# Kernel optimization log

Measured on AMD Instinct MI355X. Metric: run time of the kernel, lower is better.

Reference implementation:

```python
import jax, jax.numpy as jnp
import numpy as np

N = 50000      # nodes
E = 800000     # edges (avg degree 16)
D = 128        # d_model
C = 2          # num_classes
F_IN = 8       # GCNConv(8, d_model)


def setup_inputs() -> dict:
    key = jax.random.key(0)
    ks = jax.random.split(key, 12)
    s = 0.05  # weight init scale
    return {
        "feature_vec": jax.random.normal(ks[0], (N, F_IN), dtype=jnp.float32),
        "bboxes": jax.random.uniform(ks[1], (N, 4), dtype=jnp.float32),
        "bbox_indices": jnp.arange(N, dtype=jnp.int64) if jax.config.jax_enable_x64 else jnp.arange(N, dtype=jnp.int32),
        "edge_index": jax.random.randint(ks[2], (2, E), 0, N, dtype=jnp.int32),
        "W1": jax.random.normal(ks[3], (F_IN, D), dtype=jnp.float32) * s,
        "b1": jnp.zeros((D,), dtype=jnp.float32),
        "W2": jax.random.normal(ks[4], (D, D), dtype=jnp.float32) * s,
        "b2": jnp.zeros((D,), dtype=jnp.float32),
        "lin1_W": jax.random.normal(ks[5], (2 * D, D), dtype=jnp.float32) * s,
        "lin1_b": jnp.zeros((D,), dtype=jnp.float32),
        "linf_W": jax.random.normal(ks[6], (D, C), dtype=jnp.float32) * s,
        "linf_b": jnp.zeros((C,), dtype=jnp.float32),
    }


def gcn_conv(x, W, b, edge_index, n):
    """PyG GCNConv: add self-loops, symmetric D^-1/2 A D^-1/2 normalization."""
    x = x @ W                                   # [n, out]
    sl = jnp.arange(n, dtype=edge_index.dtype)
    row = jnp.concatenate([edge_index[0], sl])  # source
    col = jnp.concatenate([edge_index[1], sl])  # target
    ones = jnp.ones(row.shape[0], dtype=x.dtype)
    deg = jax.ops.segment_sum(ones, col, num_segments=n)  # >= 1 due to self-loops
    dinv = jax.lax.rsqrt(deg)
    norm = dinv[row] * dinv[col]                # [E + n]
    msg = x[row] * norm[:, None]                # gather + scale
    out = jax.ops.segment_sum(msg, col, num_segments=n)   # scatter-aggregate
    return out + b


def reference(feature_vec, bboxes, bbox_indices, edge_index,
              W1, b1, W2, b2, lin1_W, lin1_b, linf_W, linf_b):
    n = feature_vec.shape[0]
    x = jax.nn.relu(gcn_conv(feature_vec, W1, b1, edge_index, n))
    x = jax.nn.relu(gcn_conv(x, W2, b2, edge_index, n))
    x1 = x[edge_index[0]]                        # [E, D]
    x2 = x[edge_index[1]]                        # [E, D]
    xpair = jnp.concatenate([x1, x2], axis=-1)   # [E, 2D]
    xpair = jax.nn.relu(xpair @ lin1_W + lin1_b)
    xfin = xpair @ linf_W + linf_b               # [E, C]
    probs = jax.nn.log_softmax(xfin, axis=-1)
    bbox_pairs = jnp.concatenate([bboxes[edge_index[0]], bboxes[edge_index[1]]], axis=-1)  # [E, 8]
    bbox_index_pairs = jnp.stack([bbox_indices[edge_index[0]], bbox_indices[edge_index[1]]], axis=1)  # [E, 2]
    return (probs, bbox_pairs, bbox_index_pairs)
```

## Files before the change

kernel.cpp:

```cpp
#include <hip/hip_runtime.h>
#include <hip/hip_bf16.h>
#include <math.h>


typedef __attribute__((ext_vector_type(8))) short short8;
typedef __attribute__((ext_vector_type(4))) float f32x4;
typedef __attribute__((ext_vector_type(2))) float fv2;

__device__ inline ushort f2bf(float f) {
    union { __hip_bfloat16 h; ushort u; } cv;
    cv.h = __float2bfloat16(f);
    return cv.u;
}
__device__ inline float bf2f(ushort u) {
    union { float f; uint u; } c;
    c.u = ((uint)u) << 16;
    return c.f;
}
__device__ inline uchar f2fp8(float f) {
    uint p = __builtin_amdgcn_cvt_pk_fp8_f32(f, f, 0u, false);
    return (uchar)(p & 0xffu);
}

__global__ void k_hist(const int* __restrict__ col, int* __restrict__ cnt, int E) {
    int e = blockIdx.x * blockDim.x + threadIdx.x;
    if (e < E) atomicAdd(&cnt[col[e]], 1);
}

__global__ __launch_bounds__(1024) void k_bsum(const int* __restrict__ cnt,
                                               int* __restrict__ bsum, int N) {
    __shared__ int ts[1024];
    const int b = blockIdx.x, t = threadIdx.x;
    const int i0 = b * 2048 + 2 * t;
    int a0 = (i0 < N) ? cnt[i0] : 0;
    int a1 = (i0 + 1 < N) ? cnt[i0 + 1] : 0;
    ts[t] = a0 + a1;
    __syncthreads();
#pragma unroll
    for (int off = 512; off > 0; off >>= 1) {
        if (t < off) ts[t] += ts[t + off];
        __syncthreads();
    }
    if (t == 0) bsum[b] = ts[0];
}

__global__ __launch_bounds__(1024) void k_scanw(const int* __restrict__ cnt,
                                                const int* __restrict__ bsum,
                                                int* __restrict__ ptr, int N, int E) {
    __shared__ int ts[1024];
    const int b = blockIdx.x, t = threadIdx.x;
    int boff = 0;
    for (int i = 0; i < b; ++i) boff += bsum[i];
    const int i0 = b * 2048 + 2 * t;
    const int a0 = (i0 < N) ? cnt[i0] : 0;
    const int a1 = (i0 + 1 < N) ? cnt[i0 + 1] : 0;
    const int s = a0 + a1;
    ts[t] = s;
    __syncthreads();
    for (int off = 1; off < 1024; off <<= 1) {
        int v = (t >= off) ? ts[t - off] : 0;
        __syncthreads();
        ts[t] += v;
        __syncthreads();
    }
    const int excl = boff + ts[t] - s;
    if (i0 < N) ptr[i0] = excl;
    if (i0 + 1 < N) ptr[i0 + 1] = excl + a0;
    if (b == 0 && t == 0) ptr[N] = E;
}

__global__ void k_fill(const int* __restrict__ row, const int* __restrict__ col,
                       const int* __restrict__ cnt, const int* __restrict__ ptr,
                       int* __restrict__ cursor, int2* __restrict__ eadj, int E) {
    int e = blockIdx.x * blockDim.x + threadIdx.x;
    if (e >= E) return;
    int r = row[e], c = col[e];
    float dr = rsqrtf(1.0f + (float)cnt[r]);
    float dc = rsqrtf(1.0f + (float)cnt[c]);
    int p = ptr[c] + atomicAdd(&cursor[c], 1);
    eadj[p] = make_int2(r, __float_as_int(dr * dc));
}

__global__ void k_prepW(const float* __restrict__ lin1W, const float* __restrict__ W2,
                        ushort* __restrict__ Wuv, ushort* __restrict__ W2t) {
    int tid = blockIdx.x * blockDim.x + threadIdx.x;
    if (tid < 256 * 128) {
        int c = tid >> 7, k = tid & 127;
        int krow = k + ((c >> 7) << 7);
        Wuv[tid] = f2bf(lin1W[krow * 128 + (c & 127)]);
    } else if (tid < 256 * 128 + 128 * 128) {
        int u = tid - 256 * 128;
        int n = u >> 7, k = u & 127;
        W2t[u] = f2bf(W2[k * 128 + n]);
    }
}

__global__ __launch_bounds__(256) void k_l1(const float* __restrict__ feat,
                                            const int* __restrict__ cnt,
                                            const int* __restrict__ ptr,
                                            const int2* __restrict__ eadj,
                                            const float* __restrict__ W1,
                                            const float* __restrict__ b1,
                                            ushort* __restrict__ x1, int N) {
    __shared__ float sagg[32][8];
    __shared__ float sW1[8 * 128];
    const int tid = threadIdx.x;
    for (int i = tid; i < 1024; i += 256) sW1[i] = W1[i];

    const int lane8 = tid & 7;
    const int nloc = tid >> 3;
    const int node = blockIdx.x * 32 + nloc;
    float acc = 0.f;
    if (node < N) {
        float dd = 1.0f / (1.0f + (float)cnt[node]);
        acc = feat[(size_t)node * 8 + lane8] * dd;
        int i = ptr[node], end = ptr[node + 1];
        for (; i < end; ++i) {
            const int2 a = eadj[i];
            acc += feat[(size_t)a.x * 8 + lane8] * __int_as_float(a.y);
        }
    }
    sagg[nloc][lane8] = acc;
    __syncthreads();

    if (node < N) {
        const int jb = lane8 * 16;
        float av[8];
#pragma unroll
        for (int k = 0; k < 8; ++k) av[k] = sagg[nloc][k];
        short8 r0, r1;
#pragma unroll
        for (int j = 0; j < 16; ++j) {
            float s = b1[jb + j];
#pragma unroll
            for (int k = 0; k < 8; ++k) s = fmaf(av[k], sW1[k * 128 + jb + j], s);
            const ushort bv = f2bf(fmaxf(s, 0.f));
            if (j < 8) r0[j] = (short)bv; else r1[j - 8] = (short)bv;
        }
        *reinterpret_cast<short8*>(&x1[(size_t)node * 128 + jb]) = r0;
        *reinterpret_cast<short8*>(&x1[(size_t)node * 128 + jb + 8]) = r1;
    }
}

__global__ __launch_bounds__(256) void k_gemm2(const ushort* __restrict__ x1,
                                               const ushort* __restrict__ W2t,
                                               uchar* __restrict__ h2, int N) {
    __shared__ ushort ldsW[128 * 128];
    const int tid = threadIdx.x;
    const int wave = tid >> 6, lane = tid & 63;
    const int m = lane & 15, kb = lane >> 4;
    const int n0 = blockIdx.x * 64;

    const int node_a = min(n0 + wave * 16 + m, N - 1);
    short8 a[4];
#pragma unroll
    for (int kk = 0; kk < 4; ++kk) {
        a[kk] = *reinterpret_cast<const short8*>(&x1[(size_t)node_a * 128 + kk * 32 + kb * 8]);
    }

    {
        char* lb = reinterpret_cast<char*>(ldsW);
        const short8* wg = reinterpret_cast<const short8*>(W2t);
#pragma unroll
        for (int i = 0; i < 8; ++i) {
            const int g = i * 256 + tid;
            const int bo = g * 16;
            const int swz = bo ^ (((bo >> 8) & 7) << 4);
            *reinterpret_cast<short8*>(lb + swz) = wg[g];
        }
    }
    __syncthreads();

    f32x4 acc[8];
#pragma unroll
    for (int t = 0; t < 8; ++t) acc[t] = (f32x4){0.f, 0.f, 0.f, 0.f};

    const char* lbr = reinterpret_cast<const char*>(ldsW);
    const int mswz = (m & 7) << 4;
#pragma unroll
    for (int kk = 0; kk < 4; ++kk) {
#pragma unroll
        for (int t = 0; t < 8; ++t) {
            const int bo = (t * 16 + m) * 256 + kk * 64 + kb * 16;
            const short8 b = *reinterpret_cast<const short8*>(lbr + (bo ^ mswz));
            acc[t] = __builtin_amdgcn_mfma_f32_16x16x32_bf16(a[kk], b, acc[t], 0, 0, 0);
        }
    }

#pragma unroll
    for (int r = 0; r < 4; ++r) {
        const int node = n0 + wave * 16 + kb * 4 + r;
        if (node < N) {
#pragma unroll
            for (int t = 0; t < 8; ++t) {
                h2[(size_t)node * 128 + t * 16 + m] = f2fp8(acc[t][r]);
            }
        }
    }
}

__global__ __launch_bounds__(256) void k_gather2(const uchar* __restrict__ h2,
                                                 const int* __restrict__ cnt,
                                                 const int* __restrict__ ptr,
                                                 const int2* __restrict__ eadj,
                                                 const float* __restrict__ b2,
                                                 ushort* __restrict__ xbf, int N) {
    const int lane8 = threadIdx.x & 7;
    const int node = blockIdx.x * 32 + (threadIdx.x >> 3);
    if (node >= N) return;
    const float dd = 1.0f / (1.0f + (float)cnt[node]);
    float acc[16];
    {
        const uint4 w = *reinterpret_cast<const uint4*>(&h2[(size_t)node * 128 + lane8 * 16]);
        const uint ws[4] = {w.x, w.y, w.z, w.w};
#pragma unroll
        for (int q = 0; q < 4; ++q) {
            const fv2 lo = __builtin_amdgcn_cvt_pk_f32_fp8(ws[q], false);
            const fv2 hi = __builtin_amdgcn_cvt_pk_f32_fp8(ws[q], true);
            acc[4 * q + 0] = lo[0] * dd;
            acc[4 * q + 1] = lo[1] * dd;
            acc[4 * q + 2] = hi[0] * dd;
            acc[4 * q + 3] = hi[1] * dd;
        }
    }
    int i = ptr[node];
    const int end = ptr[node + 1];
    for (; i < end; ++i) {
        const int2 aa = eadj[i];
        const float nm = __int_as_float(aa.y);
        const uint4 w = *reinterpret_cast<const uint4*>(&h2[(size_t)aa.x * 128 + lane8 * 16]);
        const uint ws[4] = {w.x, w.y, w.z, w.w};
#pragma unroll
        for (int q = 0; q < 4; ++q) {
            const fv2 lo = __builtin_amdgcn_cvt_pk_f32_fp8(ws[q], false);
            const fv2 hi = __builtin_amdgcn_cvt_pk_f32_fp8(ws[q], true);
            acc[4 * q + 0] = fmaf(lo[0], nm, acc[4 * q + 0]);
            acc[4 * q + 1] = fmaf(lo[1], nm, acc[4 * q + 1]);
            acc[4 * q + 2] = fmaf(hi[0], nm, acc[4 * q + 2]);
            acc[4 * q + 3] = fmaf(hi[1], nm, acc[4 * q + 3]);
        }
    }
    short8 r0, r1;
#pragma unroll
    for (int q = 0; q < 8; ++q) {
        r0[q] = (short)f2bf(fmaxf(acc[q] + b2[lane8 * 16 + q], 0.f));
        r1[q] = (short)f2bf(fmaxf(acc[8 + q] + b2[lane8 * 16 + 8 + q], 0.f));
    }
    *reinterpret_cast<short8*>(&xbf[(size_t)node * 128 + lane8 * 16]) = r0;
    *reinterpret_cast<short8*>(&xbf[(size_t)node * 128 + lane8 * 16 + 8]) = r1;
}

__global__ __launch_bounds__(512) void k_gemm_uv(const ushort* __restrict__ xbf,
                                                 const ushort* __restrict__ Wuv,
                                                 const float* __restrict__ lin1b,
                                                 uchar* __restrict__ uv, int N) {
    __shared__ ushort ldsW[256 * 128];
    const int tid = threadIdx.x;
    const int wave = tid >> 6, lane = tid & 63;
    const int m = lane & 15, kb = lane >> 4;
    const int n0 = blockIdx.x * 128 + wave * 16;

    const int node_a = min(n0 + m, N - 1);
    short8 a[4];
#pragma unroll
    for (int kk = 0; kk < 4; ++kk) {
        a[kk] = *reinterpret_cast<const short8*>(&xbf[(size_t)node_a * 128 + kk * 32 + kb * 8]);
    }

    {
        char* lb = reinterpret_cast<char*>(ldsW);
        const short8* wg = reinterpret_cast<const short8*>(Wuv);
#pragma unroll
        for (int i = 0; i < 8; ++i) {
            const int g = i * 512 + tid;
            const int bo = g * 16;
            const int swz = bo ^ (((bo >> 8) & 7) << 4);
            *reinterpret_cast<short8*>(lb + swz) = wg[g];
        }
    }
    __syncthreads();

    const char* lbr = reinterpret_cast<const char*>(ldsW);
    const int mswz = (m & 7) << 4;

#pragma unroll
    for (int ch = 0; ch < 2; ++ch) {
        f32x4 acc[8];
#pragma unroll
        for (int t = 0; t < 8; ++t) acc[t] = (f32x4){0.f, 0.f, 0.f, 0.f};
#pragma unroll
        for (int kk = 0; kk < 4; ++kk) {
#pragma unroll
            for (int t = 0; t < 8; ++t) {
                const int bo = (ch * 128 + t * 16 + m) * 256 + kk * 64 + kb * 16;
                const short8 b = *reinterpret_cast<const short8*>(lbr + (bo ^ mswz));
                acc[t] = __builtin_amdgcn_mfma_f32_16x16x32_bf16(a[kk], b, acc[t], 0, 0, 0);
            }
        }
#pragma unroll
        for (int r = 0; r < 4; ++r) {
            const int node = n0 + kb * 4 + r;
            if (node < N) {
#pragma unroll
                for (int t = 0; t < 8; ++t) {
                    const int c = t * 16 + m;
                    float av = acc[t][r];
                    if (ch == 0) av += lin1b[c];
                    uv[(size_t)node * 256 + ch * 128 + c] = f2fp8(av);
                }
            }
        }
    }
}

__global__ __launch_bounds__(256) void k_edge_lite(const uchar* __restrict__ uv,
                                                   const float* __restrict__ linfW,
                                                   const float* __restrict__ linfb,
                                                   const float* __restrict__ bboxes,
                                                   const int* __restrict__ bidx,
                                                   const int* __restrict__ row,
                                                   const int* __restrict__ col,
                                                   float* __restrict__ out_probs,
                                                   float* __restrict__ out_bbox,
                                                   float* __restrict__ out_bidx,
                                                   int E) {
    const int lane8 = threadIdx.x & 7;
    const int slot = threadIdx.x >> 3;
    int e = blockIdx.x * 32 + slot;
    if (e >= E) return;

    float wd[16];
#pragma unroll
    for (int j = 0; j < 16; ++j) {
        const int c = lane8 * 16 + j;
        wd[j] = linfW[c * 2] - linfW[c * 2 + 1];
    }
    const float bias_d = linfb[0] - linfb[1];
    const int step = gridDim.x * 32;

    int s = row[e], d = col[e];
    uint4 ua = *reinterpret_cast<const uint4*>(&uv[(size_t)s * 256 + lane8 * 16]);
    uint4 va = *reinterpret_cast<const uint4*>(&uv[(size_t)d * 256 + 128 + lane8 * 16]);

    while (true) {
        const int e2 = e + step;
        const bool more = (e2 < E);
        int s2 = 0, d2 = 0;
        uint4 ua2 = ua, va2 = va;
        if (more) {
            s2 = row[e2];
            d2 = col[e2];
            ua2 = *reinterpret_cast<const uint4*>(&uv[(size_t)s2 * 256 + lane8 * 16]);
            va2 = *reinterpret_cast<const uint4*>(&uv[(size_t)d2 * 256 + 128 + lane8 * 16]);
        }

        float p = 0.f;
        {
            const uint uw[4] = {ua.x, ua.y, ua.z, ua.w};
            const uint vw[4] = {va.x, va.y, va.z, va.w};
#pragma unroll
            for (int w = 0; w < 4; ++w) {
                const fv2 ul = __builtin_amdgcn_cvt_pk_f32_fp8(uw[w], false);
                const fv2 uh = __builtin_amdgcn_cvt_pk_f32_fp8(uw[w], true);
                const fv2 vl = __builtin_amdgcn_cvt_pk_f32_fp8(vw[w], false);
                const fv2 vh = __builtin_amdgcn_cvt_pk_f32_fp8(vw[w], true);
                p = fmaf(fmaxf(ul[0] + vl[0], 0.f), wd[4 * w + 0], p);
                p = fmaf(fmaxf(ul[1] + vl[1], 0.f), wd[4 * w + 1], p);
                p = fmaf(fmaxf(uh[0] + vh[0], 0.f), wd[4 * w + 2], p);
                p = fmaf(fmaxf(uh[1] + vh[1], 0.f), wd[4 * w + 3], p);
            }
        }
        p += __shfl_xor(p, 1);
        p += __shfl_xor(p, 2);
        p += __shfl_xor(p, 4);

        out_bbox[(size_t)e * 8 + lane8] = bboxes[(size_t)((lane8 < 4) ? s : d) * 4 + (lane8 & 3)];
        if (lane8 == 0) {
            *reinterpret_cast<float2*>(&out_bidx[(size_t)e * 2]) =
                make_float2((float)bidx[s], (float)bidx[d]);
        } else if (lane8 == 1) {
            const float dd = p + bias_d;
            const float ad = fabsf(dd);
            const float t = -log1pf(expf(-ad));
            const float2 pr = (dd >= 0.f) ? make_float2(t, t - ad) : make_float2(t - ad, t);
            *reinterpret_cast<float2*>(&out_probs[(size_t)e * 2]) = pr;
        }

        if (!more) break;
        e = e2; s = s2; d = d2; ua = ua2; va = va2;
    }
}

extern "C" void kernel_launch(void* const* d_in, const int* in_sizes, int n_in,
                              void* d_out, int out_size, void* d_ws, size_t ws_size,
                              hipStream_t stream) {
    const float* feat   = (const float*)d_in[0];
    const float* bboxes = (const float*)d_in[1];
    const int*   bidx   = (const int*)d_in[2];
    const int*   eidx   = (const int*)d_in[3];
    const float* W1     = (const float*)d_in[4];
    const float* b1     = (const float*)d_in[5];
    const float* W2     = (const float*)d_in[6];
    const float* b2     = (const float*)d_in[7];
    const float* lin1W  = (const float*)d_in[8];
    const float* lin1b  = (const float*)d_in[9];
    const float* linfW  = (const float*)d_in[10];
    const float* linfb  = (const float*)d_in[11];

    const int N = in_sizes[0] / 8;
    const int E = in_sizes[3] / 2;
    const int* row = eidx;
    const int* col = eidx + E;

    size_t Np = ((size_t)N + 255) & ~255ull;
    size_t Ep = ((size_t)E + 255) & ~255ull;
    int*    cnt    = (int*)d_ws;
    int*    cursor = cnt + Np;
    int*    ptr    = cursor + Np;
    int*    bsum   = ptr + Np + 256;
    int2*   eadj   = (int2*)(bsum + 256);
    ushort* x1     = (ushort*)(eadj + Ep);
    uchar*  h2     = (uchar*)(x1 + (size_t)N * 128);
    uchar*  uvbuf  = h2 + (size_t)N * 128;
    ushort* Wuv    = (ushort*)(uvbuf + (size_t)N * 256);
    ushort* W2t    = Wuv + 256 * 128;
    ushort* xbf    = x1;

    float* out       = (float*)d_out;
    float* out_probs = out;
    float* out_bbox  = out + (size_t)E * 2;
    float* out_bidx  = out + (size_t)E * 10;

    const int B = 256;
    const int nchunk = (N + 2047) / 2048;

    hipMemsetAsync(cnt, 0, 2 * Np * sizeof(int), stream);
    k_hist<<<(E + B - 1) / B, B, 0, stream>>>(col, cnt, E);
    k_bsum<<<nchunk, 1024, 0, stream>>>(cnt, bsum, N);
    k_scanw<<<nchunk, 1024, 0, stream>>>(cnt, bsum, ptr, N, E);
    k_fill<<<(E + B - 1) / B, B, 0, stream>>>(row, col, cnt, ptr, cursor, eadj, E);
    k_prepW<<<(256 * 128 + 128 * 128 + B - 1) / B, B, 0, stream>>>(lin1W, W2, Wuv, W2t);

    k_l1<<<(N + 31) / 32, B, 0, stream>>>(feat, cnt, ptr, eadj, W1, b1, x1, N);

    k_gemm2<<<(N + 63) / 64, B, 0, stream>>>(x1, W2t, h2, N);
    k_gather2<<<(N + 31) / 32, B, 0, stream>>>(h2, cnt, ptr, eadj, b2, xbf, N);

    k_gemm_uv<<<(N + 127) / 128, 512, 0, stream>>>(xbf, Wuv, lin1b, uvbuf, N);

    k_edge_lite<<<2048, B, 0, stream>>>(uvbuf, linfW, linfb,
                                        bboxes, bidx, row, col,
                                        out_probs, out_bbox, out_bidx, E);
}
```

Baseline: 211.6 us.

## Sort nodes by in-degree to balance gather work across waves

Adds a counting sort of nodes by in-degree (histogram, scan, fill) that builds a permutation. The two neighbour-gather kernels then process nodes in degree order, so the 8-lane groups sharing a wave have similar loop lengths and less divergence. The cost is three extra small kernel launches plus atomics. Outputs stay in original node order, but memory locality of the node writes is lost.

```diff
diff --git a/kernel.cpp b/kernel.cpp
--- a/kernel.cpp
+++ b/kernel.cpp
@@ -81,6 +81,39 @@
     eadj[p] = make_int2(r, __float_as_int(dr * dc));
 }
 
+__global__ void k_dhist(const int* __restrict__ cnt, int* __restrict__ dbin, int N) {
+    int n = blockIdx.x * blockDim.x + threadIdx.x;
+    if (n < N) atomicAdd(&dbin[min(cnt[n], 255)], 1);
+}
+
+__global__ __launch_bounds__(256) void k_dscan(const int* __restrict__ dbin,
+                                               int* __restrict__ dptr,
+                                               int* __restrict__ dcur) {
+    __shared__ int ts[256];
+    const int t = threadIdx.x;
+    const int v0 = dbin[t];
+    ts[t] = v0;
+    __syncthreads();
+    for (int off = 1; off < 256; off <<= 1) {
+        int v = (t >= off) ? ts[t - off] : 0;
+        __syncthreads();
+        ts[t] += v;
+        __syncthreads();
+    }
+    const int excl = ts[t] - v0;
+    dptr[t] = excl;
+    dcur[t] = excl;
+}
+
+__global__ void k_dfill(const int* __restrict__ cnt, int* __restrict__ dcur,
+                        int* __restrict__ perm, int N) {
+    int n = blockIdx.x * blockDim.x + threadIdx.x;
+    if (n < N) {
+        int b = min(cnt[n], 255);
+        perm[atomicAdd(&dcur[b], 1)] = n;
+    }
+}
+
 __global__ void k_prepW(const float* __restrict__ lin1W, const float* __restrict__ W2,
                         ushort* __restrict__ Wuv, ushort* __restrict__ W2t) {
     int tid = blockIdx.x * blockDim.x + threadIdx.x;
@@ -99,6 +132,7 @@
                                             const int* __restrict__ cnt,
                                             const int* __restrict__ ptr,
                                             const int2* __restrict__ eadj,
+                                            const int* __restrict__ perm,
                                             const float* __restrict__ W1,
                                             const float* __restrict__ b1,
                                             ushort* __restrict__ x1, int N) {
@@ -109,9 +143,10 @@
 
     const int lane8 = tid & 7;
     const int nloc = tid >> 3;
-    const int node = blockIdx.x * 32 + nloc;
+    const int idx = blockIdx.x * 32 + nloc;
+    const int node = (idx < N) ? perm[idx] : -1;
     float acc = 0.f;
-    if (node < N) {
+    if (node >= 0) {
         float dd = 1.0f / (1.0f + (float)cnt[node]);
         acc = feat[(size_t)node * 8 + lane8] * dd;
         int i = ptr[node], end = ptr[node + 1];
@@ -123,7 +158,7 @@
     sagg[nloc][lane8] = acc;
     __syncthreads();
 
-    if (node < N) {
+    if (node >= 0) {
         const int jb = lane8 * 16;
         float av[8];
 #pragma unroll
@@ -203,11 +238,13 @@
                                                  const int* __restrict__ cnt,
                                                  const int* __restrict__ ptr,
                                                  const int2* __restrict__ eadj,
+                                                 const int* __restrict__ perm,
                                                  const float* __restrict__ b2,
                                                  ushort* __restrict__ xbf, int N) {
     const int lane8 = threadIdx.x & 7;
-    const int node = blockIdx.x * 32 + (threadIdx.x >> 3);
-    if (node >= N) return;
+    const int idx = blockIdx.x * 32 + (threadIdx.x >> 3);
+    if (idx >= N) return;
+    const int node = perm[idx];
     const float dd = 1.0f / (1.0f + (float)cnt[node]);
     float acc[16];
     {
@@ -416,9 +453,13 @@
     size_t Ep = ((size_t)E + 255) & ~255ull;
     int*    cnt    = (int*)d_ws;
     int*    cursor = cnt + Np;
-    int*    ptr    = cursor + Np;
+    int*    dbin   = cursor + Np;
+    int*    ptr    = dbin + 256;
     int*    bsum   = ptr + Np + 256;
-    int2*   eadj   = (int2*)(bsum + 256);
+    int*    dptr   = bsum + 256;
+    int*    dcur   = dptr + 256;
+    int*    perm   = dcur + 256;
+    int2*   eadj   = (int2*)(perm + Np);
     ushort* x1     = (ushort*)(eadj + Ep);
     uchar*  h2     = (uchar*)(x1 + (size_t)N * 128);
     uchar*  uvbuf  = h2 + (size_t)N * 128;
@@ -434,17 +475,20 @@
     const int B = 256;
     const int nchunk = (N + 2047) / 2048;
 
-    hipMemsetAsync(cnt, 0, 2 * Np * sizeof(int), stream);
+    hipMemsetAsync(cnt, 0, (2 * Np + 256) * sizeof(int), stream);
     k_hist<<<(E + B - 1) / B, B, 0, stream>>>(col, cnt, E);
+    k_dhist<<<(N + B - 1) / B, B, 0, stream>>>(cnt, dbin, N);
     k_bsum<<<nchunk, 1024, 0, stream>>>(cnt, bsum, N);
     k_scanw<<<nchunk, 1024, 0, stream>>>(cnt, bsum, ptr, N, E);
+    k_dscan<<<1, 256, 0, stream>>>(dbin, dptr, dcur);
+    k_dfill<<<(N + B - 1) / B, B, 0, stream>>>(cnt, dcur, perm, N);
     k_fill<<<(E + B - 1) / B, B, 0, stream>>>(row, col, cnt, ptr, cursor, eadj, E);
     k_prepW<<<(256 * 128 + 128 * 128 + B - 1) / B, B, 0, stream>>>(lin1W, W2, Wuv, W2t);
 
-    k_l1<<<(N + 31) / 32, B, 0, stream>>>(feat, cnt, ptr, eadj, W1, b1, x1, N);
+    k_l1<<<(N + 31) / 32, B, 0, stream>>>(feat, cnt, ptr, eadj, perm, W1, b1, x1, N);
 
     k_gemm2<<<(N + 63) / 64, B, 0, stream>>>(x1, W2t, h2, N);
-    k_gather2<<<(N + 31) / 32, B, 0, stream>>>(h2, cnt, ptr, eadj, b2, xbf, N);
+    k_gather2<<<(N + 31) / 32, B, 0, stream>>>(h2, cnt, ptr, eadj, perm, b2, xbf, N);
 
     k_gemm_uv<<<(N + 127) / 128, 512, 0, stream>>>(xbf, Wuv, lin1b, uvbuf, N);
 
```

New measurement: 484.1 us. +128.8%, slower.
